# Kernel tuning notes

Hardware: AMD Instinct MI355X
Metric: run time of the kernel (lower is better)

Reference implementation:

```python
import jax, jax.numpy as jnp
import numpy as np

B, N, IN_DIM, EMB, HEADS, M, ITERS = 8, 4096, 1024, 512, 4, 256, 6
DH = EMB // HEADS
SCALE = DH ** -0.5
RES_K = 33  # residual depthwise conv kernel size (TransMIL / nystrom-attention default)


def setup_inputs() -> dict:
    key = jax.random.key(0)
    ks = iter(jax.random.split(key, 40))
    def rn(shape, s=0.02):
        return jax.random.normal(next(ks), shape, jnp.float32) * s
    inp = {"X": jax.random.normal(next(ks), (B, N, IN_DIM), jnp.float32)}
    inp["few_w"] = rn((IN_DIM, EMB)); inp["few_b"] = jnp.zeros((EMB,), jnp.float32)
    inp["cls_token"] = rn((1, 1, EMB), 1.0)
    for i in (1, 2):
        inp[f"l{i}_ln_g"] = jnp.ones((EMB,), jnp.float32)
        inp[f"l{i}_ln_b"] = jnp.zeros((EMB,), jnp.float32)
        inp[f"l{i}_qkv_w"] = rn((EMB, 3 * EMB))
        inp[f"l{i}_out_w"] = rn((EMB, EMB))
        inp[f"l{i}_out_b"] = jnp.zeros((EMB,), jnp.float32)
        inp[f"l{i}_res_k"] = rn((HEADS, 1, RES_K, 1))
    for ksz in (7, 5, 3):
        inp[f"ppeg_k{ksz}"] = rn((EMB, 1, ksz, ksz))
        inp[f"ppeg_b{ksz}"] = jnp.zeros((EMB,), jnp.float32)
    inp["norm_g"] = jnp.ones((EMB,), jnp.float32)
    inp["norm_b"] = jnp.zeros((EMB,), jnp.float32)
    inp["cls_w"] = rn((EMB, 1)); inp["cls_b"] = jnp.zeros((1,), jnp.float32)
    return inp


def _ln(x, g, b):
    mu = x.mean(-1, keepdims=True)
    var = x.var(-1, keepdims=True)
    return (x - mu) / jnp.sqrt(var + 1e-5) * g + b


def _pinv(x, iters):
    # Moore-Penrose iterative pseudo-inverse of (..., m, m)
    abs_x = jnp.abs(x)
    z = jnp.swapaxes(x, -1, -2) / (abs_x.sum(-1).max() * abs_x.sum(-2).max())
    I = jnp.eye(x.shape[-1], dtype=x.dtype)
    for _ in range(iters):
        xz = x @ z
        z = 0.25 * z @ (13 * I - xz @ (15 * I - xz @ (7 * I - xz)))
    return z


def _nystrom_layer(x, ln_g, ln_b, qkv_w, out_w, out_b, res_k):
    # pre-norm transformer layer with Nystrom attention + residual depthwise conv
    b, n, d = x.shape
    h = _ln(x, ln_g, ln_b)
    pad = (-n) % M  # left-pad so seq divisible by n_landmarks
    hp = jnp.pad(h, ((0, 0), (pad, 0), (0, 0)))
    n_p = n + pad
    q, k, v = jnp.split(hp @ qkv_w, 3, axis=-1)
    def to_heads(t):
        return t.reshape(b, n_p, HEADS, DH).transpose(0, 2, 1, 3)  # (b,h,n,dh)
    q, k, v = to_heads(q) * SCALE, to_heads(k), to_heads(v)
    l = n_p // M
    q_l = q.reshape(b, HEADS, M, l, DH).mean(3)  # landmark means
    k_l = k.reshape(b, HEADS, M, l, DH).mean(3)
    a1 = jax.nn.softmax(jnp.einsum('bhid,bhjd->bhij', q, k_l), -1)    # (b,h,n,m)
    a2 = jax.nn.softmax(jnp.einsum('bhid,bhjd->bhij', q_l, k_l), -1)  # (b,h,m,m)
    a3 = jax.nn.softmax(jnp.einsum('bhid,bhjd->bhij', q_l, k), -1)    # (b,h,m,n)
    out = a1 @ (_pinv(a2, ITERS) @ (a3 @ v))
    # residual depthwise conv over sequence, one channel per head
    res = jax.lax.conv_general_dilated(
        v, res_k, (1, 1), ((RES_K // 2, RES_K // 2), (0, 0)),
        dimension_numbers=('NCHW', 'OIHW', 'NCHW'), feature_group_count=HEADS)
    out = out + res
    out = out.transpose(0, 2, 1, 3).reshape(b, n_p, d) @ out_w + out_b
    return x + out[:, -n:]


def _dwconv(x, k, bias, pad):
    y = jax.lax.conv_general_dilated(
        x, k, (1, 1), ((pad, pad), (pad, pad)),
        dimension_numbers=('NCHW', 'OIHW', 'NCHW'), feature_group_count=EMB)
    return y + bias[None, :, None, None]


def _ppeg(x, H, W, k7, b7, k5, b5, k3, b3):
    b, _, c = x.shape
    cls_t, feat = x[:, :1], x[:, 1:]
    f = feat.transpose(0, 2, 1).reshape(b, c, H, W)
    y = f + _dwconv(f, k7, b7, 3) + _dwconv(f, k5, b5, 2) + _dwconv(f, k3, b3, 1)
    y = y.reshape(b, c, H * W).transpose(0, 2, 1)
    return jnp.concatenate([cls_t, y], axis=1)


def _forward(X, few_w, few_b, cls_token,
             l1_ln_g, l1_ln_b, l1_qkv_w, l1_out_w, l1_out_b, l1_res_k,
             l2_ln_g, l2_ln_b, l2_qkv_w, l2_out_w, l2_out_b, l2_res_k,
             ppeg_k7, ppeg_b7, ppeg_k5, ppeg_b5, ppeg_k3, ppeg_b3,
             norm_g, norm_b, cls_w, cls_b):
    b, bag = X.shape[0], X.shape[1]
    h = X @ few_w + few_b
    ps = int(np.ceil(np.sqrt(bag)))
    add = ps * ps - bag
    h = jnp.concatenate([h, h[:, :add]], axis=1)  # pad bag to perfect square
    h = jnp.concatenate([jnp.broadcast_to(cls_token, (b, 1, EMB)), h], axis=1)
    h = _nystrom_layer(h, l1_ln_g, l1_ln_b, l1_qkv_w, l1_out_w, l1_out_b, l1_res_k)
    h = _ppeg(h, ps, ps, ppeg_k7, ppeg_b7, ppeg_k5, ppeg_b5, ppeg_k3, ppeg_b3)
    h = _nystrom_layer(h, l2_ln_g, l2_ln_b, l2_qkv_w, l2_out_w, l2_out_b, l2_res_k)
    h = _ln(h, norm_g, norm_b)
    return (h[:, 0] @ cls_w + cls_b).squeeze(-1)  # (batch,) bag logits


def reference(X, few_w, few_b, cls_token,
              l1_ln_g, l1_ln_b, l1_qkv_w, l1_out_w, l1_out_b, l1_res_k,
              l2_ln_g, l2_ln_b, l2_qkv_w, l2_out_w, l2_out_b, l2_res_k,
              ppeg_k7, ppeg_b7, ppeg_k5, ppeg_b5, ppeg_k3, ppeg_b3,
              norm_g, norm_b, cls_w, cls_b):
    return _forward(X, few_w, few_b, cls_token,
                    l1_ln_g, l1_ln_b, l1_qkv_w, l1_out_w, l1_out_b, l1_res_k,
                    l2_ln_g, l2_ln_b, l2_qkv_w, l2_out_w, l2_out_b, l2_res_k,
                    ppeg_k7, ppeg_b7, ppeg_k5, ppeg_b5, ppeg_k3, ppeg_b3,
                    norm_g, norm_b, cls_w, cls_b)
```

## Files before the change

### kernel.cpp

```cpp
#include <hip/hip_runtime.h>

constexpr int BATCH = 8;
constexpr int NTOK  = 4097;
constexpr int NP    = 4352;
constexpr int PADR  = 255;
constexpr int EMBD  = 512;
constexpr int DHD   = 128;
constexpr int LSUB  = 17;
constexpr float SCALE_F = 0.08838834764831845f;

constexpr int PPS   = 72;
constexpr int PPLN  = 72 * 70;
constexpr long long TPAD_FLOATS = (long long)BATCH * EMBD * PPLN;

typedef unsigned short u16;
typedef short   s16x8 __attribute__((ext_vector_type(8)));
typedef u16     u16x4 __attribute__((ext_vector_type(4)));
typedef float   f32x4 __attribute__((ext_vector_type(4)));

__device__ __forceinline__ u16 f2bf(float x) {
    unsigned u = __float_as_uint(x);
    u += 0x7fffu + ((u >> 16) & 1u);
    return (u16)(u >> 16);
}
__device__ __forceinline__ float bf2f(u16 h) {
    return __uint_as_float(((unsigned)h) << 16);
}

__device__ __forceinline__ void gload16(const u16* gp, u16* lp) {
    __builtin_amdgcn_global_load_lds(
        (const __attribute__((address_space(1))) unsigned int*)gp,
        (__attribute__((address_space(3))) unsigned int*)lp,
        16, 0, 0);
}

__device__ __forceinline__ float block_sum256(float v) {
    __shared__ float tmp[4];
    __syncthreads();
#pragma unroll
    for (int off = 32; off > 0; off >>= 1) v += __shfl_down(v, off, 64);
    int t = threadIdx.x;
    if ((t & 63) == 0) tmp[t >> 6] = v;
    __syncthreads();
    return tmp[0] + tmp[1] + tmp[2] + tmp[3];
}

__device__ __forceinline__ float block_max256(float v) {
    __shared__ float tmp[4];
    __syncthreads();
#pragma unroll
    for (int off = 32; off > 0; off >>= 1) v = fmaxf(v, __shfl_down(v, off, 64));
    int t = threadIdx.x;
    if ((t & 63) == 0) tmp[t >> 6] = v;
    __syncthreads();
    return fmaxf(fmaxf(tmp[0], tmp[1]), fmaxf(tmp[2], tmp[3]));
}

struct GemmP {
    const float* A; const float* B; float* C; const float* bias;
    long long As1, As2, Bs1, Bs2, Cs1, Cs2;
    int Adiv, Bdiv, Cdiv;
    int Am, Bk, Bn, Cm, Arow, Crow;
    int M, N, K, nb;
    float alpha; int accum;
    float bdiagc; int btrans; float cdiagc; int ctrans;
};

constexpr int LDSTR = 40;
constexpr int AH = 0, AL = 2560, BHs = 5120, BLs = 7680;

__global__ __launch_bounds__(256) void gemm_k(GemmP p) {
    __shared__ u16 lds[10240];
    const int bz = blockIdx.z;
    const float* Ab = p.A + (long long)(bz / p.Adiv) * p.As1 + (long long)(bz % p.Adiv) * p.As2;
    const float* Bb = p.B + (long long)(bz / p.Bdiv) * p.Bs1 + (long long)(bz % p.Bdiv) * p.Bs2;
    float*       Cb = p.C + (long long)(bz / p.Cdiv) * p.Cs1 + (long long)(bz % p.Cdiv) * p.Cs2;
    const int m0 = blockIdx.y * 64, n0 = blockIdx.x * 64;
    const int t = threadIdx.x;
    const int wave = t >> 6, lane = t & 63;
    const int wm = (wave & 1) * 32, wn = (wave >> 1) * 32;
    const int quad = lane >> 4, l15 = lane & 15;

    f32x4 acc[2][2];
#pragma unroll
    for (int i = 0; i < 2; ++i)
#pragma unroll
        for (int j = 0; j < 2; ++j) acc[i][j] = (f32x4){0.f, 0.f, 0.f, 0.f};

    for (int k0 = 0; k0 < p.K; k0 += 32) {
        {
            const int ar = t >> 2, ac = (t & 3) * 8;
            float v[8];
            if (m0 + ar < p.M) {
                const float* s = Ab + (long long)(m0 + ar + p.Arow) * p.Am + (k0 + ac);
                float4 x0 = *(const float4*)s, x1 = *(const float4*)(s + 4);
                v[0] = x0.x; v[1] = x0.y; v[2] = x0.z; v[3] = x0.w;
                v[4] = x1.x; v[5] = x1.y; v[6] = x1.z; v[7] = x1.w;
            } else {
#pragma unroll
                for (int i = 0; i < 8; ++i) v[i] = 0.f;
            }
            u16 h[8], l[8];
#pragma unroll
            for (int i = 0; i < 8; ++i) { h[i] = f2bf(v[i]); l[i] = f2bf(v[i] - bf2f(h[i])); }
            const int off = ar * LDSTR + ac;
            u16x4 a0, a1, b0, b1;
#pragma unroll
            for (int i = 0; i < 4; ++i) { a0[i] = h[i]; a1[i] = h[i + 4]; b0[i] = l[i]; b1[i] = l[i + 4]; }
            *(u16x4*)&lds[AH + off] = a0; *(u16x4*)&lds[AH + off + 4] = a1;
            *(u16x4*)&lds[AL + off] = b0; *(u16x4*)&lds[AL + off + 4] = b1;
        }
        if (p.Bn == 1) {
            const int bk = t >> 3, n8 = (t & 7) * 8;
            const float* s = Bb + (long long)(k0 + bk) * p.Bk + (n0 + n8);
            float4 x0 = *(const float4*)s, x1 = *(const float4*)(s + 4);
            float v[8] = {x0.x, x0.y, x0.z, x0.w, x1.x, x1.y, x1.z, x1.w};
            if (p.btrans) {
                const int gk = k0 + bk;
#pragma unroll
                for (int i = 0; i < 8; ++i)
                    v[i] = (gk == n0 + n8 + i ? p.bdiagc : 0.f) - v[i];
            }
#pragma unroll
            for (int i = 0; i < 8; ++i) {
                int j = (i + (t & 7)) & 7;
                u16 h = f2bf(v[j]);
                lds[BHs + (n8 + j) * LDSTR + bk] = h;
                lds[BLs + (n8 + j) * LDSTR + bk] = f2bf(v[j] - bf2f(h));
            }
        } else {
            const int bn = t >> 2, k8 = (t & 3) * 8;
            const float* s = Bb + (long long)(n0 + bn) * p.Bn + (k0 + k8);
            float4 x0 = *(const float4*)s, x1 = *(const float4*)(s + 4);
            float v[8] = {x0.x, x0.y, x0.z, x0.w, x1.x, x1.y, x1.z, x1.w};
            u16 h[8], l[8];
#pragma unroll
            for (int i = 0; i < 8; ++i) { h[i] = f2bf(v[i]); l[i] = f2bf(v[i] - bf2f(h[i])); }
            const int off = bn * LDSTR + k8;
            u16x4 a0, a1, b0, b1;
#pragma unroll
            for (int i = 0; i < 4; ++i) { a0[i] = h[i]; a1[i] = h[i + 4]; b0[i] = l[i]; b1[i] = l[i + 4]; }
            *(u16x4*)&lds[BHs + off] = a0; *(u16x4*)&lds[BHs + off + 4] = a1;
            *(u16x4*)&lds[BLs + off] = b0; *(u16x4*)&lds[BLs + off + 4] = b1;
        }
        __syncthreads();

        s16x8 ah[2], al[2], bh[2], bl[2];
#pragma unroll
        for (int mi = 0; mi < 2; ++mi) {
            const int off = (wm + mi * 16 + l15) * LDSTR + quad * 8;
            u16x4 q0 = *(const u16x4*)&lds[AH + off], q1 = *(const u16x4*)&lds[AH + off + 4];
            u16x4 r0 = *(const u16x4*)&lds[AL + off], r1 = *(const u16x4*)&lds[AL + off + 4];
            s16x8 fh, fl;
#pragma unroll
            for (int i = 0; i < 4; ++i) { fh[i] = q0[i]; fh[i + 4] = q1[i]; fl[i] = r0[i]; fl[i + 4] = r1[i]; }
            ah[mi] = fh; al[mi] = fl;
        }
#pragma unroll
        for (int ni = 0; ni < 2; ++ni) {
            const int off = (wn + ni * 16 + l15) * LDSTR + quad * 8;
            u16x4 q0 = *(const u16x4*)&lds[BHs + off], q1 = *(const u16x4*)&lds[BHs + off + 4];
            u16x4 r0 = *(const u16x4*)&lds[BLs + off], r1 = *(const u16x4*)&lds[BLs + off + 4];
            s16x8 fh, fl;
#pragma unroll
            for (int i = 0; i < 4; ++i) { fh[i] = q0[i]; fh[i + 4] = q1[i]; fl[i] = r0[i]; fl[i + 4] = r1[i]; }
            bh[ni] = fh; bl[ni] = fl;
        }
#pragma unroll
        for (int mi = 0; mi < 2; ++mi)
#pragma unroll
            for (int ni = 0; ni < 2; ++ni) {
                acc[mi][ni] = __builtin_amdgcn_mfma_f32_16x16x32_bf16(ah[mi], bh[ni], acc[mi][ni], 0, 0, 0);
                acc[mi][ni] = __builtin_amdgcn_mfma_f32_16x16x32_bf16(ah[mi], bl[ni], acc[mi][ni], 0, 0, 0);
                acc[mi][ni] = __builtin_amdgcn_mfma_f32_16x16x32_bf16(al[mi], bh[ni], acc[mi][ni], 0, 0, 0);
            }
        __syncthreads();
    }

#pragma unroll
    for (int mi = 0; mi < 2; ++mi)
#pragma unroll
        for (int ni = 0; ni < 2; ++ni) {
            const int n = n0 + wn + ni * 16 + l15;
#pragma unroll
            for (int r = 0; r < 4; ++r) {
                const int m = m0 + wm + mi * 16 + quad * 4 + r;
                if (m >= p.M) continue;
                float v = p.alpha * acc[mi][ni][r];
                if (p.bias) v += p.bias[n];
                if (p.ctrans) v = (m == n ? p.cdiagc : 0.f) - v;
                float* dst = Cb + (long long)(m + p.Crow) * p.Cm + n;
                if (p.accum) *dst += v; else *dst = v;
            }
        }
}

struct SplitP {
    const float* src; u16* dh; u16* dl;
    long long s1, s2, rstride, dstride, total;
    int div, R, C8;
    float scale;
};
__global__ __launch_bounds__(256) void split_k(SplitP p) {
    long long idx = (long long)blockIdx.x * 256 + threadIdx.x;
    if (idx >= p.total) return;
    int c8 = (int)(idx % p.C8);
    long long tmp = idx / p.C8;
    int r  = (int)(tmp % p.R);
    int bz = (int)(tmp / p.R);
    const float* s = p.src + (long long)(bz / p.div) * p.s1 + (long long)(bz % p.div) * p.s2
                   + (long long)r * p.rstride + c8 * 8;
    float4 x0 = *(const float4*)s, x1 = *(const float4*)(s + 4);
    float v[8] = {x0.x, x0.y, x0.z, x0.w, x1.x, x1.y, x1.z, x1.w};
    s16x8 hv, lv;
#pragma unroll
    for (int i = 0; i < 8; ++i) {
        float sv = v[i] * p.scale;
        u16 h = f2bf(sv);
        hv[i] = (short)h;
        lv[i] = (short)f2bf(sv - bf2f(h));
    }
    long long doff = (long long)bz * p.dstride + (long long)r * (p.C8 * 8) + c8 * 8;
    *(s16x8*)&p.dh[doff] = hv;
    *(s16x8*)&p.dl[doff] = lv;
}

__global__ __launch_bounds__(256) void splitT_k(const float* __restrict__ src,
                                                u16* __restrict__ dh, u16* __restrict__ dl,
                                                int K, int N) {
    int idx = blockIdx.x * 256 + threadIdx.x;
    if (idx >= N * K) return;
    int n = idx / K, k = idx - n * K;
    float v = src[(long long)k * N + n];
    u16 h = f2bf(v);
    dh[idx] = h;
    dl[idx] = f2bf(v - bf2f(h));
}

struct GemmBtP {
    const u16 *Ah, *Al, *Bh, *Bl;
    float* C; const float* bias;
    long long Abs, Bbs, Cbs;
    int M, N, K, Cm, Crow, accum;
};

__global__ __launch_bounds__(512, 4) void gemm_bt_k(GemmBtP p) {
    __shared__ __align__(16) u16 lds[16384];
    const int bz = blockIdx.z;
    const u16* Ahb = p.Ah + (long long)bz * p.Abs;
    const u16* Alb = p.Al + (long long)bz * p.Abs;
    const u16* Bhb = p.Bh + (long long)bz * p.Bbs;
    const u16* Blb = p.Bl + (long long)bz * p.Bbs;
    float*     Cb  = p.C  + (long long)bz * p.Cbs;

    const int NX = gridDim.x;
    const int nwg = NX * gridDim.y;
    const int bid = blockIdx.y * NX + blockIdx.x;
    const int qq = nwg >> 3, rr = nwg & 7;
    const int xcd = bid & 7, loc = bid >> 3;
    const int nbid = (xcd < rr) ? (xcd * (qq + 1) + loc)
                                : (rr * (qq + 1) + (xcd - rr) * qq + loc);
    const int m0 = (nbid / NX) * 128, n0 = (nbid % NX) * 256;

    const int t = threadIdx.x;
    const int wave = t >> 6, lane = t & 63;
    const int wm = (wave & 1) * 64, wn = (wave >> 1) * 64;
    const int quad = lane >> 4, l15 = lane & 15;
    const int K = p.K;

    const int srow = 16 * wave + (lane >> 2);
    const int sga  = (m0 + srow < p.M) ? (m0 + srow) : (p.M - 1);
    const long long sbase = (long long)sga * K + (lane & 3) * 8;
    u16* ldsw = &lds[wave * 512];

    const long long bb0   = (long long)(n0 + wn + l15) * K + quad * 8;
    const long long bstep = 16LL * K;

    f32x4 acc[4][4];
#pragma unroll
    for (int i = 0; i < 4; ++i)
#pragma unroll
        for (int j = 0; j < 4; ++j) acc[i][j] = (f32x4){0.f, 0.f, 0.f, 0.f};

    gload16(Ahb + sbase, ldsw);
    gload16(Alb + sbase, ldsw + 4096);
    __syncthreads();

    const int nt = K >> 5;
    int cur = 0;
    for (int t0 = 0; t0 < nt; ++t0) {
        const int k0 = t0 << 5;
        s16x8 bh[4], bl[4];
#pragma unroll
        for (int ni = 0; ni < 4; ++ni) {
            const long long bo = bb0 + ni * bstep + k0;
            bh[ni] = *(const s16x8*)&Bhb[bo];
            bl[ni] = *(const s16x8*)&Blb[bo];
        }
        if (t0 + 1 < nt) {
            u16* dst = ldsw + (cur ^ 1) * 8192;
            gload16(Ahb + sbase + k0 + 32, dst);
            gload16(Alb + sbase + k0 + 32, dst + 4096);
        }
        const int bufo = cur * 8192;
#pragma unroll
        for (int mi = 0; mi < 4; ++mi) {
            const int off = bufo + (wm + mi * 16 + l15) * 32 + quad * 8;
            s16x8 ah = *(const s16x8*)&lds[off];
            s16x8 al = *(const s16x8*)&lds[off + 4096];
#pragma unroll
            for (int ni = 0; ni < 4; ++ni) {
                acc[mi][ni] = __builtin_amdgcn_mfma_f32_16x16x32_bf16(ah, bh[ni], acc[mi][ni], 0, 0, 0);
                acc[mi][ni] = __builtin_amdgcn_mfma_f32_16x16x32_bf16(ah, bl[ni], acc[mi][ni], 0, 0, 0);
                acc[mi][ni] = __builtin_amdgcn_mfma_f32_16x16x32_bf16(al, bh[ni], acc[mi][ni], 0, 0, 0);
            }
        }
        __syncthreads();
        cur ^= 1;
    }

#pragma unroll
    for (int mi = 0; mi < 4; ++mi)
#pragma unroll
        for (int ni = 0; ni < 4; ++ni) {
            const int n = n0 + wn + ni * 16 + l15;
            const float bv = p.bias ? p.bias[n] : 0.f;
#pragma unroll
            for (int r = 0; r < 4; ++r) {
                const int m = m0 + wm + mi * 16 + quad * 4 + r;
                if (m >= p.M) continue;
                float* dst = Cb + (long long)(m + p.Crow) * p.Cm + n;
                float v = acc[mi][ni][r] + bv;
                if (p.accum) *dst += v; else *dst = v;
            }
        }
}

__global__ void cls_set_k(float* H0, const float* cls) {
    int t = blockIdx.x * 256 + threadIdx.x;
    int b = t >> 9, c = t & 511;
    H0[(long long)b * NTOK * EMBD + c] = cls[c];
}

__global__ __launch_bounds__(256) void ln_pad_k(const float* __restrict__ H0,
                                                u16* __restrict__ oh, u16* __restrict__ ol,
                                                const float* g, const float* bb) {
    int row = blockIdx.x, b = blockIdx.y, t = threadIdx.x;
    long long off = ((long long)b * NP + row) * EMBD;
    if (row < PADR) {
        oh[off + t] = 0; oh[off + t + 256] = 0;
        ol[off + t] = 0; ol[off + t + 256] = 0;
        return;
    }
    const float* x = H0 + ((long long)b * NTOK + (row - PADR)) * EMBD;
    float v0 = x[t], v1 = x[t + 256];
    float mu = block_sum256(v0 + v1) * (1.f / EMBD);
    float d0 = v0 - mu, d1 = v1 - mu;
    float var = block_sum256(d0 * d0 + d1 * d1) * (1.f / EMBD);
    float rs = 1.f / sqrtf(var + 1e-5f);
    float y0 = d0 * rs * g[t]       + bb[t];
    float y1 = d1 * rs * g[t + 256] + bb[t + 256];
    u16 h0 = f2bf(y0); oh[off + t]       = h0; ol[off + t]       = f2bf(y0 - bf2f(h0));
    u16 h1 = f2bf(y1); oh[off + t + 256] = h1; ol[off + t + 256] = f2bf(y1 - bf2f(h1));
}

__global__ void landmark_k(const float* __restrict__ QKV, float* __restrict__ QL,
                           float* __restrict__ KL) {
    long long idx = (long long)blockIdx.x * 256 + threadIdx.x;
    int d = idx & 127; int i = (int)((idx >> 7) & 255); int bh = (int)(idx >> 15);
    int b = bh >> 2, h = bh & 3;
    const float* base = QKV + (long long)b * NP * 1536 + (long long)i * LSUB * 1536 + h * DHD + d;
    float sq = 0.f, sk = 0.f;
#pragma unroll
    for (int j = 0; j < LSUB; ++j) { sq += base[j * 1536]; sk += base[j * 1536 + EMBD]; }
    QL[idx] = sq * (1.f / LSUB);
    KL[idx] = sk * (1.f / LSUB);
}

__global__ __launch_bounds__(256) void softmax256_k(float* __restrict__ X) {
    long long row = (long long)blockIdx.x * 4 + (threadIdx.x >> 6);
    int lane = threadIdx.x & 63;
    float4* p = (float4*)(X + row * 256) + lane;
    float4 v = *p;
    float m = fmaxf(fmaxf(v.x, v.y), fmaxf(v.z, v.w));
#pragma unroll
    for (int off = 32; off > 0; off >>= 1) m = fmaxf(m, __shfl_xor(m, off, 64));
    float ex = __expf(v.x - m), ey = __expf(v.y - m), ez = __expf(v.z - m), ew = __expf(v.w - m);
    float s = ex + ey + ez + ew;
#pragma unroll
    for (int off = 32; off > 0; off >>= 1) s += __shfl_xor(s, off, 64);
    float inv = 1.f / s;
    *p = make_float4(ex * inv, ey * inv, ez * inv, ew * inv);
}

__global__ __launch_bounds__(256) void softmax_lds_k(float* __restrict__ X) {
    __shared__ float rowbuf[4352];
    float4* p  = (float4*)(X + (long long)blockIdx.x * 4352);
    float4* r4 = (float4*)rowbuf;
    const int t = threadIdx.x;
    float m = -1e30f;
    for (int i = t; i < 1088; i += 256) {
        float4 v = p[i]; r4[i] = v;
        m = fmaxf(m, fmaxf(fmaxf(v.x, v.y), fmaxf(v.z, v.w)));
    }
    m = block_max256(m);
    float s = 0.f;
    for (int i = t; i < 1088; i += 256) {
        float4 v = r4[i];
        v.x = __expf(v.x - m); v.y = __expf(v.y - m); v.z = __expf(v.z - m); v.w = __expf(v.w - m);
        r4[i] = v;
        s += v.x + v.y + v.z + v.w;
    }
    s = block_sum256(s);
    float inv = 1.f / s;
    for (int i = t; i < 1088; i += 256) {
        float4 v = r4[i];
        p[i] = make_float4(v.x * inv, v.y * inv, v.z * inv, v.w * inv);
    }
}

__global__ __launch_bounds__(256) void pinv_absmax_k(const float* __restrict__ X, float* red) {
    int bh = blockIdx.x, t = threadIdx.x;
    const float* x = X + (long long)bh * 65536;
    float rs = 0.f, cs = 0.f;
    for (int j = 0; j < 256; ++j) { rs += fabsf(x[t * 256 + j]); cs += fabsf(x[j * 256 + t]); }
    float mr = block_max256(rs);
    float mc = block_max256(cs);
    if (t == 0) { red[bh] = mr; red[32 + bh] = mc; }
}

__global__ void pinv_scalar_k(const float* red, float* inv) {
    float mr = 0.f, mc = 0.f;
    for (int i = 0; i < 32; ++i) { mr = fmaxf(mr, red[i]); mc = fmaxf(mc, red[32 + i]); }
    inv[0] = 1.f / (mr * mc);
}

__global__ void pinv_tinit_k(const float* __restrict__ X, const float* __restrict__ inv,
                             float* __restrict__ Z) {
    long long idx = (long long)blockIdx.x * 256 + threadIdx.x;
    int j = (int)(idx & 255); int i = (int)((idx >> 8) & 255); long long bh = idx >> 16;
    Z[idx] = X[(bh << 16) + ((long long)j << 8) + i] * inv[0];
}

__global__ void resconv_k(const float* __restrict__ QKV, const float* __restrict__ rk,
                          float* __restrict__ ATT2) {
    long long idx = (long long)blockIdx.x * 256 + threadIdx.x;
    if (idx >= (long long)BATCH * NTOK * EMBD) return;
    int c = (int)(idx & 511); long long r = idx >> 9;
    int n = PADR + (int)(r % NTOK); int b = (int)(r / NTOK);
    int h = c >> 7, d = c & 127;
    const float* vb = QKV + (long long)b * NP * 1536 + 1024 + h * DHD + d;
    float acc = 0.f;
#pragma unroll
    for (int u = 0; u < 33; ++u) {
        int nn = n + u - 16;
        if (nn >= 0 && nn < NP) acc += vb[(long long)nn * 1536] * rk[h * 33 + u];
    }
    ATT2[((long long)b * NP + n) * EMBD + c] += acc;
}

__global__ void wsum_k(const float* __restrict__ k7, const float* __restrict__ k5,
                       const float* __restrict__ k3, const float* __restrict__ b7,
                       const float* __restrict__ b5, const float* __restrict__ b3,
                       float* __restrict__ W) {
    int idx = blockIdx.x * 256 + threadIdx.x;
    if (idx < 25088) {
        int c = idx / 49, i = idx - c * 49;
        int dy = i / 7, dx = i - dy * 7;
        float w = k7[idx];
        if (dy >= 1 && dy <= 5 && dx >= 1 && dx <= 5) w += k5[c * 25 + (dy - 1) * 5 + (dx - 1)];
        if (dy >= 2 && dy <= 4 && dx >= 2 && dx <= 4) w += k3[c * 9 + (dy - 2) * 3 + (dx - 2)];
        W[idx] = w;
    } else if (idx < 25600) {
        int c = idx - 25088;
        W[25088 + c] = b7[c] + b5[c] + b3[c];
    }
}

__global__ __launch_bounds__(256) void tin_k(const float* __restrict__ H0,
                                             float* __restrict__ Tpad) {
    __shared__ float lds[64][65];
    const int y = blockIdx.x, c0 = blockIdx.y * 64, b = blockIdx.z;
    const int t = threadIdx.x;
    const int pc = t & 63, pr4 = t >> 6;
    const float* src = H0 + ((long long)b * NTOK + 1 + y * 64) * EMBD + c0;
#pragma unroll
    for (int i = 0; i < 16; ++i) {
        int pr = pr4 + i * 4;
        lds[pr][pc] = src[(long long)pr * EMBD + pc];
    }
    __syncthreads();
    const int xw = t & 63, cw4 = t >> 6;
#pragma unroll
    for (int i = 0; i < 16; ++i) {
        int cw = cw4 + i * 4;
        Tpad[(long long)(b * 512 + c0 + cw) * PPLN + (3 + y) * PPS + 3 + xw] = lds[xw][cw];
    }
}

__global__ __launch_bounds__(256, 4) void conv7_k(const float* __restrict__ Tpad,
                                                  const float* __restrict__ Wall,
                                                  float* __restrict__ Tout) {
    const int bc = blockIdx.x;
    const int c = bc & 511;
    const int t = threadIdx.x;
    const int x = t & 63, band = t >> 6;
    const int y0 = band * 16;
    const float* in = Tpad + (long long)bc * PPLN + x;
    float* outp = Tout + (long long)bc * 4096 + x;

    float W[49];
#pragma unroll
    for (int i = 0; i < 49; ++i) W[i] = Wall[c * 49 + i];
    const float bias = Wall[25088 + c];

    float win[7][7];
#pragma unroll
    for (int j = 0; j < 6; ++j)
#pragma unroll
        for (int d = 0; d < 7; ++d)
            win[j][d] = in[(y0 + j) * PPS + d];

#pragma unroll
    for (int yy = 0; yy < 16; ++yy) {
        const int slot = (6 + yy) % 7;
#pragma unroll
        for (int d = 0; d < 7; ++d)
            win[slot][d] = in[(y0 + yy + 6) * PPS + d];
        float s = bias + win[(yy + 3) % 7][3];
#pragma unroll
        for (int dy = 0; dy < 7; ++dy) {
            const int r = (yy + dy) % 7;
#pragma unroll
            for (int dx = 0; dx < 7; ++dx)
                s += W[dy * 7 + dx] * win[r][dx];
        }
        outp[(y0 + yy) * 64] = s;
    }
}

__global__ __launch_bounds__(256) void tout_k(const float* __restrict__ Tout,
                                              float* __restrict__ H0) {
    __shared__ float lds[64][65];
    const int y = blockIdx.x, c0 = blockIdx.y * 64, b = blockIdx.z;
    const int t = threadIdx.x;
    const int xl = t & 63, cl4 = t >> 6;
#pragma unroll
    for (int i = 0; i < 16; ++i) {
        int cl = cl4 + i * 4;
        lds[xl][cl] = Tout[(long long)(b * 512 + c0 + cl) * 4096 + y * 64 + xl];
    }
    __syncthreads();
    const int pc = t & 63, pl4 = t >> 6;
    float* dst = H0 + ((long long)b * NTOK + 1 + y * 64) * EMBD + c0;
#pragma unroll
    for (int i = 0; i < 16; ++i) {
        int pl = pl4 + i * 4;
        dst[(long long)pl * EMBD + pc] = lds[pl][pc];
    }
}

__global__ __launch_bounds__(256) void head_k(const float* __restrict__ H0, const float* g,
                                              const float* bb, const float* cw, const float* cb,
                                              float* __restrict__ out) {
    int b = blockIdx.x, t = threadIdx.x;
    const float* x = H0 + (long long)b * NTOK * EMBD;
    float v0 = x[t], v1 = x[t + 256];
    float mu = block_sum256(v0 + v1) * (1.f / EMBD);
    float d0 = v0 - mu, d1 = v1 - mu;
    float var = block_sum256(d0 * d0 + d1 * d1) * (1.f / EMBD);
    float rs = 1.f / sqrtf(var + 1e-5f);
    float y0 = d0 * rs * g[t] + bb[t];
    float y1 = d1 * rs * g[t + 256] + bb[t + 256];
    float s = block_sum256(y0 * cw[t] + y1 * cw[t + 256]);
    if (t == 0) out[b] = s + cb[0];
}

extern "C" void kernel_launch(void* const* d_in, const int* in_sizes, int n_in,
                              void* d_out, int out_size, void* d_ws, size_t ws_size,
                              hipStream_t stream) {
    (void)in_sizes; (void)n_in; (void)out_size; (void)ws_size;
    const float* X        = (const float*)d_in[0];
    const float* few_w    = (const float*)d_in[1];
    const float* few_b    = (const float*)d_in[2];
    const float* cls_tok  = (const float*)d_in[3];
    const float* ln_g[2]  = {(const float*)d_in[4],  (const float*)d_in[10]};
    const float* ln_b[2]  = {(const float*)d_in[5],  (const float*)d_in[11]};
    const float* qkv_w[2] = {(const float*)d_in[6],  (const float*)d_in[12]};
    const float* out_w[2] = {(const float*)d_in[7],  (const float*)d_in[13]};
    const float* out_b[2] = {(const float*)d_in[8],  (const float*)d_in[14]};
    const float* res_k[2] = {(const float*)d_in[9],  (const float*)d_in[15]};
    const float* k7 = (const float*)d_in[16]; const float* b7 = (const float*)d_in[17];
    const float* k5 = (const float*)d_in[18]; const float* b5 = (const float*)d_in[19];
    const float* k3 = (const float*)d_in[20]; const float* b3 = (const float*)d_in[21];
    const float* norm_g = (const float*)d_in[22]; const float* norm_b = (const float*)d_in[23];
    const float* cls_w  = (const float*)d_in[24]; const float* cls_b  = (const float*)d_in[25];
    float* out = (float*)d_out;

    float* ws  = (float*)d_ws;
    float* H0  = ws;
    float* LNH = H0  + 16781312LL;
    float* QKV = LNH + 17825792LL;
    float* A3  = QKV + 53477376LL;
    float* QL  = A3  + 35651584LL;
    float* KL  = QL  + 1048576LL;
    float* A2  = KL  + 1048576LL;
    float* KV  = A2  + 2097152LL;
    float* ZKV = KV  + 1048576LL;
    float* RED = ZKV + 1048576LL;

    u16* LNHh = (u16*)LNH;
    u16* LNHl = (u16*)(LNH + 8912896LL);
    u16* QLh  = (u16*)KV;
    u16* QLl  = (u16*)(KV + 524288LL);
    u16* KLh  = (u16*)ZKV;
    u16* KLl  = (u16*)(ZKV + 524288LL);
    u16* Xh   = (u16*)A3;
    u16* Xl   = (u16*)(A3 + 16777216LL);
    u16* ATh  = (u16*)A3;
    u16* ATl  = (u16*)(A3 + 8390656LL);
    u16* Wh   = (u16*)A2;
    u16* fwl  = (u16*)(A2 + 262144LL);
    u16* qwl  = (u16*)(A2 + 393216LL);
    u16* owl  = (u16*)(A2 + 131072LL);
    float* Zb0 = LNH;
    float* Zb1 = LNH + 2097152LL;
    float* XZm = LNH + 4194304LL;
    float* U1  = LNH + 6291456LL;
    float* U2  = LNH + 8388608LL;
    float* Tpad = QKV;
    float* Tout = QKV + TPAD_FLOATS;
    float* WSUM = A3;

    auto gemmx = [&](const float* A, long long As1, long long As2, int Adiv, int Am, int Arow,
                     const float* Bm, long long Bs1, long long Bs2, int Bdiv, int Bk, int Bn,
                     float* C, long long Cs1, long long Cs2, int Cdiv, int Cm, int Crow,
                     int M, int N, int K, int nb, float alpha, int accum, const float* bias,
                     float bdiagc, int btrans, float cdiagc, int ctrans) {
        GemmP p;
        p.A = A; p.B = Bm; p.C = C; p.bias = bias;
        p.As1 = As1; p.As2 = As2; p.Bs1 = Bs1; p.Bs2 = Bs2; p.Cs1 = Cs1; p.Cs2 = Cs2;
        p.Adiv = Adiv; p.Bdiv = Bdiv; p.Cdiv = Cdiv;
        p.Am = Am; p.Bk = Bk; p.Bn = Bn; p.Cm = Cm; p.Arow = Arow; p.Crow = Crow;
        p.M = M; p.N = N; p.K = K; p.nb = nb; p.alpha = alpha; p.accum = accum;
        p.bdiagc = bdiagc; p.btrans = btrans; p.cdiagc = cdiagc; p.ctrans = ctrans;
        dim3 grid(N / 64, (M + 63) / 64, nb);
        gemm_k<<<grid, 256, 0, stream>>>(p);
    };
    auto gemm = [&](const float* A, long long As1, long long As2, int Adiv, int Am, int Arow,
                    const float* Bm, long long Bs1, long long Bs2, int Bdiv, int Bk, int Bn,
                    float* C, long long Cs1, long long Cs2, int Cdiv, int Cm, int Crow,
                    int M, int N, int K, int nb, float alpha, int accum, const float* bias) {
        gemmx(A, As1, As2, Adiv, Am, Arow, Bm, Bs1, Bs2, Bdiv, Bk, Bn,
              C, Cs1, Cs2, Cdiv, Cm, Crow, M, N, K, nb, alpha, accum, bias, 0.f, 0, 0.f, 0);
    };
    auto split = [&](const float* src, u16* dh, u16* dl, long long s1, long long s2, int div,
                     long long rstride, int R, int C, int nb, float scale) {
        SplitP p;
        p.src = src; p.dh = dh; p.dl = dl;
        p.s1 = s1; p.s2 = s2; p.div = div;
        p.rstride = rstride; p.R = R; p.C8 = C >> 3;
        p.dstride = (long long)R * C;
        p.total = (long long)nb * R * (C >> 3);
        p.scale = scale;
        int blocks = (int)((p.total + 255) / 256);
        split_k<<<blocks, 256, 0, stream>>>(p);
    };
    auto gemmbt = [&](const u16* Ah, const u16* Al, long long Abs,
                      const u16* Bh, const u16* Bl, long long Bbs,
                      float* C, long long Cbs, int Cm, int Crow,
                      int M, int N, int K, int nb, int accum, const float* bias) {
        GemmBtP p;
        p.Ah = Ah; p.Al = Al; p.Bh = Bh; p.Bl = Bl;
        p.C = C; p.bias = bias;
        p.Abs = Abs; p.Bbs = Bbs; p.Cbs = Cbs;
        p.M = M; p.N = N; p.K = K; p.Cm = Cm; p.Crow = Crow; p.accum = accum;
        dim3 grid(N / 256, (M + 127) / 128, nb);
        gemm_bt_k<<<grid, 512, 0, stream>>>(p);
    };

    cls_set_k<<<16, 256, 0, stream>>>(H0, cls_tok);
    split(X, Xh, Xl, 0, 0, 1, 1024, 32768, 1024, 1, 1.f);
    splitT_k<<<2048, 256, 0, stream>>>(few_w, Wh, fwl, 1024, 512);
    gemmbt(Xh, Xl, 4194304LL, Wh, fwl, 0,
           H0, 2097664LL, 512, 1,
           4096, 512, 1024, BATCH, 0, few_b);

    for (int L = 0; L < 2; ++L) {
        ln_pad_k<<<dim3(NP, BATCH), 256, 0, stream>>>(H0, LNHh, LNHl, ln_g[L], ln_b[L]);
        splitT_k<<<3072, 256, 0, stream>>>(qkv_w[L], Wh, qwl, 512, 1536);
        gemmbt(LNHh, LNHl, 0, Wh, qwl, 0,
               QKV, 0, 1536, 0,
               34816, 1536, 512, 1, 0, nullptr);
        landmark_k<<<4096, 256, 0, stream>>>(QKV, QL, KL);
        gemm(QL, 32768LL, 0, 1, 128, 0,
             KL, 32768LL, 0, 1, 1, 128,
             A2, 65536LL, 0, 1, 256, 0,
             256, 256, 128, 32, SCALE_F, 0, nullptr);
        softmax256_k<<<2048, 256, 0, stream>>>(A2);
        split(QL, QLh, QLl, 32768LL, 0, 1, 128, 256, 128, 32, SCALE_F);
        split(KL, KLh, KLl, 32768LL, 0, 1, 128, 256, 128, 32, 1.f);
        split(QKV + 512, LNHh, LNHl, 6680064LL, 128LL, 4, 1536, 4352, 128, 32, 1.f);
        gemmbt(QLh, QLl, 32768LL, LNHh, LNHl, 557056LL,
               A3, 1114112LL, 4352, 0,
               256, 4352, 128, 32, 0, nullptr);
        softmax_lds_k<<<8192, 256, 0, stream>>>(A3);
        gemm(A3, 1114112LL, 0, 1, 4352, 0,
             QKV + 1024, 6680064LL, 128LL, 4, 1536, 1,
             KV, 32768LL, 0, 1, 128, 0,
             256, 128, 4352, 32, 1.f, 0, nullptr);
        split(QKV, LNHh, LNHl, 6680064LL, 128LL, 4, 1536, 4352, 128, 32, SCALE_F);
        gemmbt(LNHh, LNHl, 557056LL, KLh, KLl, 32768LL,
               A3, 1114112LL, 256, 0,
               4352, 256, 128, 32, 0, nullptr);
        softmax256_k<<<34816, 256, 0, stream>>>(A3);
        pinv_absmax_k<<<32, 256, 0, stream>>>(A2, RED);
        pinv_scalar_k<<<1, 1, 0, stream>>>(RED, RED + 64);
        pinv_tinit_k<<<8192, 256, 0, stream>>>(A2, RED + 64, Zb0);
        float* zc = Zb0; float* zn = Zb1;
        for (int it = 0; it < 6; ++it) {
            gemm(A2, 65536LL, 0, 1, 256, 0, zc, 65536LL, 0, 1, 256, 1,
                 XZm, 65536LL, 0, 1, 256, 0, 256, 256, 256, 32, 1.f, 0, nullptr);
            gemmx(XZm, 65536LL, 0, 1, 256, 0, XZm, 65536LL, 0, 1, 256, 1,
                  U1, 65536LL, 0, 1, 256, 0, 256, 256, 256, 32, 1.f, 0, nullptr,
                  7.f, 1, 15.f, 1);
            gemmx(XZm, 65536LL, 0, 1, 256, 0, U1, 65536LL, 0, 1, 256, 1,
                  U2, 65536LL, 0, 1, 256, 0, 256, 256, 256, 32, 1.f, 0, nullptr,
                  0.f, 0, 13.f, 1);
            gemm(zc, 65536LL, 0, 1, 256, 0, U2, 65536LL, 0, 1, 256, 1,
                 zn, 65536LL, 0, 1, 256, 0, 256, 256, 256, 32, 0.25f, 0, nullptr);
            float* t2 = zc; zc = zn; zn = t2;
        }
        gemm(zc, 65536LL, 0, 1, 256, 0,
             KV, 32768LL, 0, 1, 128, 1,
             ZKV, 32768LL, 0, 1, 128, 0,
             256, 128, 256, 32, 1.f, 0, nullptr);
        gemm(A3, 1114112LL, 0, 1, 256, 0,
             ZKV, 32768LL, 0, 1, 128, 1,
             LNH, 2228224LL, 128LL, 4, 512, 0,
             4352, 128, 256, 32, 1.f, 0, nullptr);
        resconv_k<<<65552, 256, 0, stream>>>(QKV, res_k[L], LNH);
        split(LNH + PADR * 512, ATh, ATl, 2228224LL, 0, 1, 512, 4097, 512, 8, 1.f);
        splitT_k<<<1024, 256, 0, stream>>>(out_w[L], Wh, owl, 512, 512);
        gemmbt(ATh, ATl, 2097664LL, Wh, owl, 0,
               H0, 2097664LL, 512, 0,
               4097, 512, 512, BATCH, 1, out_b[L]);

        if (L == 0) {
            hipMemsetAsync(Tpad, 0, TPAD_FLOATS * sizeof(float), stream);
            wsum_k<<<101, 256, 0, stream>>>(k7, k5, k3, b7, b5, b3, WSUM);
            tin_k<<<dim3(64, 8, 8), 256, 0, stream>>>(H0, Tpad);
            conv7_k<<<4096, 256, 0, stream>>>(Tpad, WSUM, Tout);
            tout_k<<<dim3(64, 8, 8), 256, 0, stream>>>(Tout, H0);
        }
    }

    head_k<<<BATCH, 256, 0, stream>>>(H0, norm_g, norm_b, cls_w, cls_b, out);
}
```

Before: 4.323 ms.

## Run pseudo-inverse iterations on split-bf16 MFMA GEMMs with fused epilogues

Replaces the fp32 generic GEMMs in the 6-iteration Moore-Penrose pseudo-inverse loop, and the final Z@KV product, with a dedicated 256-wide MFMA kernel. It uses hi/lo bf16 splitting with three MFMAs per step to emulate fp32 precision. The epilogue writes the outputs already split into bf16 pairs, in both normal and transposed layouts, and folds the (c*I - X) diagonal terms into the store. This removes the separate split and transpose passes between GEMMs. It drops the low*low product term, which costs a little accuracy, and the kernel reads operands straight from global memory without LDS staging.

```diff
diff --git a/kernel.cpp b/kernel.cpp
--- a/kernel.cpp
+++ b/kernel.cpp
@@ -237,6 +237,16 @@
     dl[idx] = f2bf(v - bf2f(h));
 }
 
+__global__ void splitTb_k(const float* __restrict__ KV, u16* __restrict__ dh,
+                          u16* __restrict__ dl) {
+    long long idx = (long long)blockIdx.x * 256 + threadIdx.x;
+    int k = (int)(idx & 255); int n = (int)((idx >> 8) & 127); long long bh = idx >> 15;
+    float v = KV[(bh << 15) + ((long long)k << 7) + n];
+    u16 h = f2bf(v);
+    dh[idx] = h;
+    dl[idx] = f2bf(v - bf2f(h));
+}
+
 struct GemmBtP {
     const u16 *Ah, *Al, *Bh, *Bl;
     float* C; const float* bias;
@@ -332,6 +342,82 @@
                 float* dst = Cb + (long long)(m + p.Crow) * p.Cm + n;
                 float v = acc[mi][ni][r] + bv;
                 if (p.accum) *dst += v; else *dst = v;
+            }
+        }
+}
+
+struct GemmPsP {
+    const u16 *Ah, *Al, *Bh, *Bl;
+    float* Cf; u16 *CNh, *CNl, *CTh, *CTl;
+    long long CfS;
+    int N;
+    float alpha; int ctrans; float cdiag; int ctsub; float ctdiag;
+};
+
+__global__ __launch_bounds__(256) void gemm_ps_k(GemmPsP p) {
+    const int bz = blockIdx.z;
+    const long long ab = (long long)bz << 16;
+    const long long bb = (long long)bz * ((long long)p.N << 8);
+    const u16* Ah = p.Ah + ab; const u16* Al = p.Al + ab;
+    const u16* Bh = p.Bh + bb; const u16* Bl = p.Bl + bb;
+    const int m0 = blockIdx.y * 64, n0 = blockIdx.x * 64;
+    const int t = threadIdx.x;
+    const int wave = t >> 6, lane = t & 63;
+    const int wm = (wave & 1) * 32, wn = (wave >> 1) * 32;
+    const int quad = lane >> 4, l15 = lane & 15;
+
+    f32x4 acc[2][2];
+#pragma unroll
+    for (int i = 0; i < 2; ++i)
+#pragma unroll
+        for (int j = 0; j < 2; ++j) acc[i][j] = (f32x4){0.f, 0.f, 0.f, 0.f};
+
+    const int ar = (m0 + wm + l15) * 256 + quad * 8;
+    const int br = (n0 + wn + l15) * 256 + quad * 8;
+    for (int k0 = 0; k0 < 256; k0 += 32) {
+        s16x8 ah[2], aw[2], bh[2], bl[2];
+#pragma unroll
+        for (int mi = 0; mi < 2; ++mi) {
+            ah[mi] = *(const s16x8*)&Ah[ar + mi * 4096 + k0];
+            aw[mi] = *(const s16x8*)&Al[ar + mi * 4096 + k0];
+        }
+#pragma unroll
+        for (int ni = 0; ni < 2; ++ni) {
+            bh[ni] = *(const s16x8*)&Bh[br + ni * 4096 + k0];
+            bl[ni] = *(const s16x8*)&Bl[br + ni * 4096 + k0];
+        }
+#pragma unroll
+        for (int mi = 0; mi < 2; ++mi)
+#pragma unroll
+            for (int ni = 0; ni < 2; ++ni) {
+                acc[mi][ni] = __builtin_amdgcn_mfma_f32_16x16x32_bf16(ah[mi], bh[ni], acc[mi][ni], 0, 0, 0);
+                acc[mi][ni] = __builtin_amdgcn_mfma_f32_16x16x32_bf16(ah[mi], bl[ni], acc[mi][ni], 0, 0, 0);
+                acc[mi][ni] = __builtin_amdgcn_mfma_f32_16x16x32_bf16(aw[mi], bh[ni], acc[mi][ni], 0, 0, 0);
+            }
+    }
+
+#pragma unroll
+    for (int mi = 0; mi < 2; ++mi)
+#pragma unroll
+        for (int ni = 0; ni < 2; ++ni) {
+            const int n = n0 + wn + ni * 16 + l15;
+#pragma unroll
+            for (int r = 0; r < 4; ++r) {
+                const int m = m0 + wm + mi * 16 + quad * 4 + r;
+                float v = p.alpha * acc[mi][ni][r];
+                if (p.ctrans) v = (m == n ? p.cdiag : 0.f) - v;
+                if (p.Cf) p.Cf[(long long)bz * p.CfS + (long long)m * p.N + n] = v;
+                if (p.CNh) {
+                    u16 h = f2bf(v);
+                    p.CNh[ab + m * 256 + n] = h;
+                    p.CNl[ab + m * 256 + n] = f2bf(v - bf2f(h));
+                }
+                if (p.CTh) {
+                    float w = p.ctsub ? ((m == n ? p.ctdiag : 0.f) - v) : v;
+                    u16 h = f2bf(w);
+                    p.CTh[bb + n * 256 + m] = h;
+                    p.CTl[bb + n * 256 + m] = f2bf(w - bf2f(h));
+                }
             }
         }
 }
@@ -435,11 +521,16 @@
     inv[0] = 1.f / (mr * mc);
 }
 
-__global__ void pinv_tinit_k(const float* __restrict__ X, const float* __restrict__ inv,
-                             float* __restrict__ Z) {
+__global__ void tinit2_k(const float* __restrict__ X, const float* __restrict__ inv,
+                         u16* __restrict__ Zsh, u16* __restrict__ Zsl,
+                         u16* __restrict__ Zth, u16* __restrict__ Ztl) {
     long long idx = (long long)blockIdx.x * 256 + threadIdx.x;
-    int j = (int)(idx & 255); int i = (int)((idx >> 8) & 255); long long bh = idx >> 16;
-    Z[idx] = X[(bh << 16) + ((long long)j << 8) + i] * inv[0];
+    int c = (int)(idx & 255); int r = (int)((idx >> 8) & 255); long long bh = idx >> 16;
+    float v = X[idx] * inv[0];
+    u16 h = f2bf(v), l = f2bf(v - bf2f(h));
+    Zth[idx] = h; Ztl[idx] = l;
+    long long zs = (bh << 16) + ((long long)c << 8) + r;
+    Zsh[zs] = h; Zsl[zs] = l;
 }
 
 __global__ void resconv_k(const float* __restrict__ QKV, const float* __restrict__ rk,
@@ -623,11 +714,6 @@
     u16* fwl  = (u16*)(A2 + 262144LL);
     u16* qwl  = (u16*)(A2 + 393216LL);
     u16* owl  = (u16*)(A2 + 131072LL);
-    float* Zb0 = LNH;
-    float* Zb1 = LNH + 2097152LL;
-    float* XZm = LNH + 4194304LL;
-    float* U1  = LNH + 6291456LL;
-    float* U2  = LNH + 8388608LL;
     float* Tpad = QKV;
     float* Tout = QKV + TPAD_FLOATS;
     float* WSUM = A3;
@@ -678,6 +764,18 @@
         dim3 grid(N / 256, (M + 127) / 128, nb);
         gemm_bt_k<<<grid, 512, 0, stream>>>(p);
     };
+    auto gps = [&](const u16* Ah, const u16* Al, const u16* Bh, const u16* Bl,
+                   float* Cf, long long CfS, int N,
+                   u16* CNh, u16* CNl, u16* CTh, u16* CTl,
+                   float alpha, int ctrans, float cdiag, int ctsub, float ctdiag) {
+        GemmPsP q;
+        q.Ah = Ah; q.Al = Al; q.Bh = Bh; q.Bl = Bl;
+        q.Cf = Cf; q.CNh = CNh; q.CNl = CNl; q.CTh = CTh; q.CTl = CTl;
+        q.CfS = CfS; q.N = N;
+        q.alpha = alpha; q.ctrans = ctrans; q.cdiag = cdiag;
+        q.ctsub = ctsub; q.ctdiag = ctdiag;
+        gemm_ps_k<<<dim3(N / 64, 4, 32), 256, 0, stream>>>(q);
+    };
 
     cls_set_k<<<16, 256, 0, stream>>>(H0, cls_tok);
     split(X, Xh, Xl, 0, 0, 1, 1024, 32768, 1024, 1, 1.f);
@@ -714,27 +812,37 @@
                A3, 1114112LL, 256, 0,
                4352, 256, 128, 32, 0, nullptr);
         softmax256_k<<<34816, 256, 0, stream>>>(A3);
+
+        auto PP = [&](int i){ return (u16*)(LNH + (long long)i * 2097152LL); };
+        u16 *A2sh = PP(0), *A2sl = PP(0) + 2097152;
+        u16 *Zsh[2] = {PP(1), PP(3)}, *Zsl[2] = {PP(1) + 2097152, PP(3) + 2097152};
+        u16 *Zth[2] = {PP(2), PP(4)}, *Ztl[2] = {PP(2) + 2097152, PP(4) + 2097152};
+        u16 *XZh = PP(5), *XZl = PP(5) + 2097152;
+        u16 *Tah = PP(6), *Tal = PP(6) + 2097152;
+        u16 *Tbh = PP(7), *Tbl = PP(7) + 2097152;
+        u16 *KVth = (u16*)(LNH + 16777216LL), *KVtl = KVth + 1048576;
+
+        split(A2, A2sh, A2sl, 65536LL, 0, 1, 256, 256, 256, 32, 1.f);
         pinv_absmax_k<<<32, 256, 0, stream>>>(A2, RED);
         pinv_scalar_k<<<1, 1, 0, stream>>>(RED, RED + 64);
-        pinv_tinit_k<<<8192, 256, 0, stream>>>(A2, RED + 64, Zb0);
-        float* zc = Zb0; float* zn = Zb1;
+        tinit2_k<<<8192, 256, 0, stream>>>(A2, RED + 64, Zsh[0], Zsl[0], Zth[0], Ztl[0]);
+        int cur = 0;
         for (int it = 0; it < 6; ++it) {
-            gemm(A2, 65536LL, 0, 1, 256, 0, zc, 65536LL, 0, 1, 256, 1,
-                 XZm, 65536LL, 0, 1, 256, 0, 256, 256, 256, 32, 1.f, 0, nullptr);
-            gemmx(XZm, 65536LL, 0, 1, 256, 0, XZm, 65536LL, 0, 1, 256, 1,
-                  U1, 65536LL, 0, 1, 256, 0, 256, 256, 256, 32, 1.f, 0, nullptr,
-                  7.f, 1, 15.f, 1);
-            gemmx(XZm, 65536LL, 0, 1, 256, 0, U1, 65536LL, 0, 1, 256, 1,
-                  U2, 65536LL, 0, 1, 256, 0, 256, 256, 256, 32, 1.f, 0, nullptr,
-                  0.f, 0, 13.f, 1);
-            gemm(zc, 65536LL, 0, 1, 256, 0, U2, 65536LL, 0, 1, 256, 1,
-                 zn, 65536LL, 0, 1, 256, 0, 256, 256, 256, 32, 0.25f, 0, nullptr);
-            float* t2 = zc; zc = zn; zn = t2;
-        }
-        gemm(zc, 65536LL, 0, 1, 256, 0,
-             KV, 32768LL, 0, 1, 128, 1,
-             ZKV, 32768LL, 0, 1, 128, 0,
-             256, 128, 256, 32, 1.f, 0, nullptr);
+            gps(A2sh, A2sl, Zth[cur], Ztl[cur], nullptr, 0, 256,
+                XZh, XZl, Tah, Tal, 1.f, 0, 0.f, 1, 7.f);
+            gps(XZh, XZl, Tah, Tal, nullptr, 0, 256,
+                nullptr, nullptr, Tbh, Tbl, 1.f, 1, 15.f, 0, 0.f);
+            gps(XZh, XZl, Tbh, Tbl, nullptr, 0, 256,
+                nullptr, nullptr, Tah, Tal, 1.f, 1, 13.f, 0, 0.f);
+            gps(Zsh[cur], Zsl[cur], Tah, Tal, nullptr, 0, 256,
+                Zsh[cur ^ 1], Zsl[cur ^ 1], Zth[cur ^ 1], Ztl[cur ^ 1],
+                0.25f, 0, 0.f, 0, 0.f);
+            cur ^= 1;
+        }
+        splitTb_k<<<4096, 256, 0, stream>>>(KV, KVth, KVtl);
+        gps(Zsh[cur], Zsl[cur], KVth, KVtl, ZKV, 32768LL, 128,
+            nullptr, nullptr, nullptr, nullptr, 1.f, 0, 0.f, 0, 0.f);
+
         gemm(A3, 1114112LL, 0, 1, 256, 0,
              ZKV, 32768LL, 0, 1, 128, 1,
              LNH, 2228224LL, 128LL, 4, 512, 0,
```

Result: slower. 4.616 ms (+6.8%).

## Fuse row softmax into Q·Klᵀ GEMM epilogue and fold bf16 splits into producers

Applied to the files above, without the earlier changes.

Adds an optional softmax epilogue to the split-bf16 GEMM. Each 256-wide output row is normalized in registers using shuffles and an LDS cross-wave reduction, which removes a separate softmax pass over the 4352x256 attention matrix. The landmark kernel now emits the hi/lo bf16 splits of the scaled Q and K landmarks directly, and the residual-conv kernel writes hi/lo bf16 attention output instead of accumulating into fp32 and then calling split. This cuts several full-tensor read/write passes and kernel launches, at the cost of extra epilogue work and barriers inside the GEMM.

```diff
diff --git a/kernel.cpp b/kernel.cpp
--- a/kernel.cpp
+++ b/kernel.cpp
@@ -241,7 +241,7 @@
     const u16 *Ah, *Al, *Bh, *Bl;
     float* C; const float* bias;
     long long Abs, Bbs, Cbs;
-    int M, N, K, Cm, Crow, accum;
+    int M, N, K, Cm, Crow, accum, smax;
 };
 
 __global__ __launch_bounds__(512, 4) void gemm_bt_k(GemmBtP p) {
@@ -317,6 +317,60 @@
         }
         __syncthreads();
         cur ^= 1;
+    }
+
+    if (p.smax) {
+        float* sred = (float*)lds;
+        const int wg = wn >> 6;
+        float rmax[4][4];
+#pragma unroll
+        for (int mi = 0; mi < 4; ++mi)
+#pragma unroll
+            for (int r = 0; r < 4; ++r) {
+                float pm = fmaxf(fmaxf(acc[mi][0][r], acc[mi][1][r]),
+                                 fmaxf(acc[mi][2][r], acc[mi][3][r]));
+#pragma unroll
+                for (int off = 8; off > 0; off >>= 1)
+                    pm = fmaxf(pm, __shfl_xor(pm, off, 64));
+                if (l15 == 0) sred[(wm + mi * 16 + quad * 4 + r) * 4 + wg] = pm;
+            }
+        __syncthreads();
+#pragma unroll
+        for (int mi = 0; mi < 4; ++mi)
+#pragma unroll
+            for (int r = 0; r < 4; ++r) {
+                const int row = wm + mi * 16 + quad * 4 + r;
+                rmax[mi][r] = fmaxf(fmaxf(sred[row * 4 + 0], sred[row * 4 + 1]),
+                                    fmaxf(sred[row * 4 + 2], sred[row * 4 + 3]));
+            }
+        __syncthreads();
+#pragma unroll
+        for (int mi = 0; mi < 4; ++mi)
+#pragma unroll
+            for (int r = 0; r < 4; ++r) {
+                float s = 0.f;
+#pragma unroll
+                for (int ni = 0; ni < 4; ++ni) {
+                    float e = __expf(acc[mi][ni][r] - rmax[mi][r]);
+                    acc[mi][ni][r] = e;
+                    s += e;
+                }
+#pragma unroll
+                for (int off = 8; off > 0; off >>= 1)
+                    s += __shfl_xor(s, off, 64);
+                if (l15 == 0) sred[(wm + mi * 16 + quad * 4 + r) * 4 + wg] = s;
+            }
+        __syncthreads();
+#pragma unroll
+        for (int mi = 0; mi < 4; ++mi)
+#pragma unroll
+            for (int r = 0; r < 4; ++r) {
+                const int row = wm + mi * 16 + quad * 4 + r;
+                float inv = 1.f / (sred[row * 4 + 0] + sred[row * 4 + 1] +
+                                   sred[row * 4 + 2] + sred[row * 4 + 3]);
+#pragma unroll
+                for (int ni = 0; ni < 4; ++ni) acc[mi][ni][r] *= inv;
+            }
     }
 
 #pragma unroll
@@ -365,7 +419,9 @@
 }
 
 __global__ void landmark_k(const float* __restrict__ QKV, float* __restrict__ QL,
-                           float* __restrict__ KL) {
+                           float* __restrict__ KL,
+                           u16* __restrict__ qh, u16* __restrict__ qlo,
+                           u16* __restrict__ kh, u16* __restrict__ klo) {
     long long idx = (long long)blockIdx.x * 256 + threadIdx.x;
     int d = idx & 127; int i = (int)((idx >> 7) & 255); int bh = (int)(idx >> 15);
     int b = bh >> 2, h = bh & 3;
@@ -373,8 +429,13 @@
     float sq = 0.f, sk = 0.f;
 #pragma unroll
     for (int j = 0; j < LSUB; ++j) { sq += base[j * 1536]; sk += base[j * 1536 + EMBD]; }
-    QL[idx] = sq * (1.f / LSUB);
-    KL[idx] = sk * (1.f / LSUB);
+    float q = sq * (1.f / LSUB);
+    float k = sk * (1.f / LSUB);
+    QL[idx] = q;
+    KL[idx] = k;
+    float qs = q * SCALE_F;
+    u16 h1 = f2bf(qs); qh[idx] = h1; qlo[idx] = f2bf(qs - bf2f(h1));
+    u16 h2 = f2bf(k);  kh[idx] = h2; klo[idx] = f2bf(k - bf2f(h2));
 }
 
 __global__ __launch_bounds__(256) void softmax256_k(float* __restrict__ X) {
@@ -443,11 +504,13 @@
 }
 
 __global__ void resconv_k(const float* __restrict__ QKV, const float* __restrict__ rk,
-                          float* __restrict__ ATT2) {
+                          const float* __restrict__ ATT2,
+                          u16* __restrict__ ath, u16* __restrict__ atl) {
     long long idx = (long long)blockIdx.x * 256 + threadIdx.x;
     if (idx >= (long long)BATCH * NTOK * EMBD) return;
     int c = (int)(idx & 511); long long r = idx >> 9;
-    int n = PADR + (int)(r % NTOK); int b = (int)(r / NTOK);
+    int rr = (int)(r % NTOK); int b = (int)(r / NTOK);
+    int n = PADR + rr;
     int h = c >> 7, d = c & 127;
     const float* vb = QKV + (long long)b * NP * 1536 + 1024 + h * DHD + d;
     float acc = 0.f;
@@ -456,7 +519,11 @@
         int nn = n + u - 16;
         if (nn >= 0 && nn < NP) acc += vb[(long long)nn * 1536] * rk[h * 33 + u];
     }
-    ATT2[((long long)b * NP + n) * EMBD + c] += acc;
+    float fin = ATT2[((long long)b * NP + n) * EMBD + c] + acc;
+    long long didx = (long long)b * 2097664LL + (long long)rr * 512 + c;
+    u16 hh = f2bf(fin);
+    ath[didx] = hh;
+    atl[didx] = f2bf(fin - bf2f(hh));
 }
 
 __global__ void wsum_k(const float* __restrict__ k7, const float* __restrict__ k5,
@@ -669,12 +736,13 @@
     auto gemmbt = [&](const u16* Ah, const u16* Al, long long Abs,
                       const u16* Bh, const u16* Bl, long long Bbs,
                       float* C, long long Cbs, int Cm, int Crow,
-                      int M, int N, int K, int nb, int accum, const float* bias) {
+                      int M, int N, int K, int nb, int accum, const float* bias, int smax) {
         GemmBtP p;
         p.Ah = Ah; p.Al = Al; p.Bh = Bh; p.Bl = Bl;
         p.C = C; p.bias = bias;
         p.Abs = Abs; p.Bbs = Bbs; p.Cbs = Cbs;
         p.M = M; p.N = N; p.K = K; p.Cm = Cm; p.Crow = Crow; p.accum = accum;
+        p.smax = smax;
         dim3 grid(N / 256, (M + 127) / 128, nb);
         gemm_bt_k<<<grid, 512, 0, stream>>>(p);
     };
@@ -684,26 +752,24 @@
     splitT_k<<<2048, 256, 0, stream>>>(few_w, Wh, fwl, 1024, 512);
     gemmbt(Xh, Xl, 4194304LL, Wh, fwl, 0,
            H0, 2097664LL, 512, 1,
-           4096, 512, 1024, BATCH, 0, few_b);
+           4096, 512, 1024, BATCH, 0, few_b, 0);
 
     for (int L = 0; L < 2; ++L) {
         ln_pad_k<<<dim3(NP, BATCH), 256, 0, stream>>>(H0, LNHh, LNHl, ln_g[L], ln_b[L]);
         splitT_k<<<3072, 256, 0, stream>>>(qkv_w[L], Wh, qwl, 512, 1536);
         gemmbt(LNHh, LNHl, 0, Wh, qwl, 0,
                QKV, 0, 1536, 0,
-               34816, 1536, 512, 1, 0, nullptr);
-        landmark_k<<<4096, 256, 0, stream>>>(QKV, QL, KL);
+               34816, 1536, 512, 1, 0, nullptr, 0);
+        landmark_k<<<4096, 256, 0, stream>>>(QKV, QL, KL, QLh, QLl, KLh, KLl);
         gemm(QL, 32768LL, 0, 1, 128, 0,
              KL, 32768LL, 0, 1, 1, 128,
              A2, 65536LL, 0, 1, 256, 0,
              256, 256, 128, 32, SCALE_F, 0, nullptr);
         softmax256_k<<<2048, 256, 0, stream>>>(A2);
-        split(QL, QLh, QLl, 32768LL, 0, 1, 128, 256, 128, 32, SCALE_F);
-        split(KL, KLh, KLl, 32768LL, 0, 1, 128, 256, 128, 32, 1.f);
         split(QKV + 512, LNHh, LNHl, 6680064LL, 128LL, 4, 1536, 4352, 128, 32, 1.f);
         gemmbt(QLh, QLl, 32768LL, LNHh, LNHl, 557056LL,
                A3, 1114112LL, 4352, 0,
-               256, 4352, 128, 32, 0, nullptr);
+               256, 4352, 128, 32, 0, nullptr, 0);
         softmax_lds_k<<<8192, 256, 0, stream>>>(A3);
         gemm(A3, 1114112LL, 0, 1, 4352, 0,
              QKV + 1024, 6680064LL, 128LL, 4, 1536, 1,
@@ -712,8 +778,7 @@
         split(QKV, LNHh, LNHl, 6680064LL, 128LL, 4, 1536, 4352, 128, 32, SCALE_F);
         gemmbt(LNHh, LNHl, 557056LL, KLh, KLl, 32768LL,
                A3, 1114112LL, 256, 0,
-               4352, 256, 128, 32, 0, nullptr);
-        softmax256_k<<<34816, 256, 0, stream>>>(A3);
+               4352, 256, 128, 32, 0, nullptr, 1);
         pinv_absmax_k<<<32, 256, 0, stream>>>(A2, RED);
         pinv_scalar_k<<<1, 1, 0, stream>>>(RED, RED + 64);
         pinv_tinit_k<<<8192, 256, 0, stream>>>(A2, RED + 64, Zb0);
@@ -739,12 +804,11 @@
              ZKV, 32768LL, 0, 1, 128, 1,
              LNH, 2228224LL, 128LL, 4, 512, 0,
              4352, 128, 256, 32, 1.f, 0, nullptr);
-        resconv_k<<<65552, 256, 0, stream>>>(QKV, res_k[L], LNH);
-        split(LNH + PADR * 512, ATh, ATl, 2228224LL, 0, 1, 512, 4097, 512, 8, 1.f);
+        resconv_k<<<65552, 256, 0, stream>>>(QKV, res_k[L], LNH, ATh, ATl);
         splitT_k<<<1024, 256, 0, stream>>>(out_w[L], Wh, owl, 512, 512);
         gemmbt(ATh, ATl, 2097664LL, Wh, owl, 0,
                H0, 2097664LL, 512, 0,
-               4097, 512, 512, BATCH, 1, out_b[L]);
+               4097, 512, 512, BATCH, 1, out_b[L], 0);
 
         if (L == 0) {
             hipMemsetAsync(Tpad, 0, TPAD_FLOATS * sizeof(float), stream);
```

Measured after the change: 4.375 ms. About the same (+1.2%).
